# Optimization experiments

Hardware: AMD Instinct MI355X
Metric: run time of the kernel (lower is better)

The kernel has to match this reference:

```python
import jax, jax.numpy as jnp
import numpy as np


def setup_inputs() -> dict:
    key = jax.random.key(0)
    k1, k2 = jax.random.split(key)
    X = jax.random.normal(k1, (8192, 10000), dtype=jnp.float32)
    # logits parameter, xavier_normal init: std = sqrt(2/(fan_in+fan_out))
    std = np.sqrt(2.0 / (256 + 10000)).astype(np.float32)
    logits = jax.random.normal(k2, (256, 10000), dtype=jnp.float32) * std
    return {"X": X, "logits": logits, "temp": 1}


def reference(X, logits, temp):
    # Gumbel-softmax with hard=True (straight-through), matching F.gumbel_softmax.
    gkey = jax.random.key(42)
    g = jax.random.gumbel(gkey, logits.shape, dtype=logits.dtype)
    y_soft = jax.nn.softmax((logits + g) / temp, axis=-1)          # [S, D]
    idx = jnp.argmax(y_soft, axis=-1)                               # [S]
    y_hard = jax.nn.one_hot(idx, logits.shape[-1], dtype=y_soft.dtype)
    # hard forward, soft backward: y_hard - sg(y_soft) + y_soft
    selections = y_hard - jax.lax.stop_gradient(y_soft) + y_soft    # [S, D]
    # Y = X @ selections^T  (one-hot rows -> column gather of X)
    Y = jnp.matmul(X, selections.T)                                 # [B, S]
    return Y
```

## Files before the change

### kernel.cpp

```cpp
#include <hip/hip_runtime.h>
#include <stdint.h>

#define PRNG_VARIANT 1

#define S_ROWS 256
#define D_COLS 10000
#define B_ROWS 8192
#define HALF_N 1280000u

__device__ __forceinline__ void threefry2x32(uint32_t& x0, uint32_t& x1) {
  const uint32_t k0 = 0u;
  const uint32_t k1 = 42u;
  const uint32_t k2 = 0x1BD11BDAu ^ k0 ^ k1;
  x0 += k0; x1 += k1;
#define TFR(r) { x0 += x1; x1 = (x1 << (r)) | (x1 >> (32 - (r))); x1 ^= x0; }
  TFR(13) TFR(15) TFR(26) TFR(6)   x0 += k1; x1 += k2 + 1u;
  TFR(17) TFR(29) TFR(16) TFR(24)  x0 += k2; x1 += k0 + 2u;
  TFR(13) TFR(15) TFR(26) TFR(6)   x0 += k0; x1 += k1 + 3u;
  TFR(17) TFR(29) TFR(16) TFR(24)  x0 += k1; x1 += k2 + 4u;
  TFR(13) TFR(15) TFR(26) TFR(6)   x0 += k2; x1 += k0 + 5u;
#undef TFR
}

__device__ __forceinline__ uint32_t jax_random_bits(uint32_t i) {
#if PRNG_VARIANT == 0
  uint32_t x0, x1;
  if (i < HALF_N) { x0 = i; x1 = i + HALF_N; }
  else            { x0 = i - HALF_N; x1 = i; }
  threefry2x32(x0, x1);
  return (i < HALF_N) ? x0 : x1;
#else
  uint32_t x0 = 0u;
  uint32_t x1 = i;
  threefry2x32(x0, x1);
#if PRNG_VARIANT == 2
  return x0;
#elif PRNG_VARIANT == 3
  return x1;
#else
  return x0 ^ x1;
#endif
#endif
}

__device__ __forceinline__ double gumbel_from_bits(uint32_t bits) {
  uint32_t fb = (bits >> 9) | 0x3f800000u;
  float u = __uint_as_float(fb) - 1.0f;
  if (u <= 0.0f) u = 1.17549435e-38f;
  double lu = log((double)u);
  return -log(-lu);
}

__global__ __launch_bounds__(256)
void argmax_gumbel_kernel(const float* __restrict__ logits, int* __restrict__ idx_out) {
  const int s   = blockIdx.x;
  const int tid = threadIdx.x;

  double best = -1.0e300;
  int    bi   = 0;
  const int base = s * D_COLS;
  for (int d = tid; d < D_COLS; d += 256) {
    uint32_t bits = jax_random_bits((uint32_t)(base + d));
    double z = (double)logits[base + d] + gumbel_from_bits(bits);
    if (z > best) { best = z; bi = d; }
  }

  __shared__ double sv[256];
  __shared__ int    si[256];
  sv[tid] = best; si[tid] = bi;
  __syncthreads();
  for (int off = 128; off > 0; off >>= 1) {
    if (tid < off) {
      double ov = sv[tid + off]; int oi = si[tid + off];
      if (ov > sv[tid] || (ov == sv[tid] && oi < si[tid])) { sv[tid] = ov; si[tid] = oi; }
    }
    __syncthreads();
  }
  if (tid == 0) idx_out[s] = si[0];
}

#define ROWS_PER_BLOCK 16
__global__ __launch_bounds__(256)
void gather_cols_kernel(const float* __restrict__ X,
                        const int* __restrict__ idx,
                        float* __restrict__ Y) {
  const int s   = threadIdx.x;
  const int col = idx[s];
  const long b0 = (long)blockIdx.x * ROWS_PER_BLOCK;
#pragma unroll
  for (int r = 0; r < ROWS_PER_BLOCK; ++r) {
    const long b = b0 + r;
    Y[b * S_ROWS + s] = X[b * D_COLS + col];
  }
}

extern "C" void kernel_launch(void* const* d_in, const int* in_sizes, int n_in,
                              void* d_out, int out_size, void* d_ws, size_t ws_size,
                              hipStream_t stream) {
  const float* X      = (const float*)d_in[0];
  const float* logits = (const float*)d_in[1];
  float*       Y      = (float*)d_out;
  int*         idx    = (int*)d_ws;

  argmax_gumbel_kernel<<<S_ROWS, 256, 0, stream>>>(logits, idx);
  gather_cols_kernel<<<B_ROWS / ROWS_PER_BLOCK, 256, 0, stream>>>(X, idx, Y);
}
```

Measured before the change: 436.9 us.

## Use float Gumbel argmax with double-precision candidate rescoring, wider blocks

The argmax kernel now computes Gumbel noise with float logf instead of double log, buffers z values in shared memory, and rescores in double only the candidates within a small threshold of the float maximum. Blocks grow to 1024 threads. The gather kernel halves rows per block and separates loads from stores to raise memory-level parallelism. Exactness relies on the threshold covering float error, and the serial rescoring is capped at 64 candidates.

```diff
diff --git a/kernel.cpp b/kernel.cpp
--- a/kernel.cpp
+++ b/kernel.cpp
@@ -1,12 +1,10 @@
 #include <hip/hip_runtime.h>
 #include <stdint.h>
 
-#define PRNG_VARIANT 1
 
 #define S_ROWS 256
 #define D_COLS 10000
 #define B_ROWS 8192
-#define HALF_N 1280000u
 
 __device__ __forceinline__ void threefry2x32(uint32_t& x0, uint32_t& x1) {
   const uint32_t k0 = 0u;
@@ -23,63 +21,88 @@
 }
 
 __device__ __forceinline__ uint32_t jax_random_bits(uint32_t i) {
-#if PRNG_VARIANT == 0
-  uint32_t x0, x1;
-  if (i < HALF_N) { x0 = i; x1 = i + HALF_N; }
-  else            { x0 = i - HALF_N; x1 = i; }
+  uint32_t x0 = 0u, x1 = i;
   threefry2x32(x0, x1);
-  return (i < HALF_N) ? x0 : x1;
-#else
-  uint32_t x0 = 0u;
-  uint32_t x1 = i;
-  threefry2x32(x0, x1);
-#if PRNG_VARIANT == 2
-  return x0;
-#elif PRNG_VARIANT == 3
-  return x1;
-#else
   return x0 ^ x1;
-#endif
-#endif
 }
 
-__device__ __forceinline__ double gumbel_from_bits(uint32_t bits) {
+__device__ __forceinline__ float uniform_from_bits(uint32_t bits) {
   uint32_t fb = (bits >> 9) | 0x3f800000u;
   float u = __uint_as_float(fb) - 1.0f;
   if (u <= 0.0f) u = 1.17549435e-38f;
+  return u;
+}
+
+__device__ __forceinline__ float gumbel_f(uint32_t bits) {
+  float u  = uniform_from_bits(bits);
+  float nl = -logf(u);
+  return -logf(nl);
+}
+
+__device__ __forceinline__ double gumbel_d(uint32_t bits) {
+  float u = uniform_from_bits(bits);
   double lu = log((double)u);
   return -log(-lu);
 }
 
-__global__ __launch_bounds__(256)
+#define ARGMAX_THREADS 1024
+#define CAND_MAX 64
+
+__global__ __launch_bounds__(ARGMAX_THREADS)
 void argmax_gumbel_kernel(const float* __restrict__ logits, int* __restrict__ idx_out) {
   const int s   = blockIdx.x;
   const int tid = threadIdx.x;
+  const int base = s * D_COLS;
 
-  double best = -1.0e300;
-  int    bi   = 0;
-  const int base = s * D_COLS;
-  for (int d = tid; d < D_COLS; d += 256) {
+  __shared__ float zbuf[D_COLS];
+  __shared__ float sv[ARGMAX_THREADS];
+  __shared__ int   si[ARGMAX_THREADS];
+  __shared__ int   n_cand;
+  __shared__ int   cand[CAND_MAX];
+
+  if (tid == 0) n_cand = 0;
+
+  float best = -1.0e30f;
+  int   bi   = 0;
+  for (int d = tid; d < D_COLS; d += ARGMAX_THREADS) {
     uint32_t bits = jax_random_bits((uint32_t)(base + d));
-    double z = (double)logits[base + d] + gumbel_from_bits(bits);
+    float z = logits[base + d] + gumbel_f(bits);
+    zbuf[d] = z;
     if (z > best) { best = z; bi = d; }
   }
-
-  __shared__ double sv[256];
-  __shared__ int    si[256];
   sv[tid] = best; si[tid] = bi;
   __syncthreads();
-  for (int off = 128; off > 0; off >>= 1) {
+  for (int off = ARGMAX_THREADS / 2; off > 0; off >>= 1) {
     if (tid < off) {
-      double ov = sv[tid + off]; int oi = si[tid + off];
+      float ov = sv[tid + off]; int oi = si[tid + off];
       if (ov > sv[tid] || (ov == sv[tid] && oi < si[tid])) { sv[tid] = ov; si[tid] = oi; }
     }
     __syncthreads();
   }
-  if (tid == 0) idx_out[s] = si[0];
+
+  const float thresh = sv[0] - 1.0e-3f;
+  for (int d = tid; d < D_COLS; d += ARGMAX_THREADS) {
+    if (zbuf[d] >= thresh) {
+      int pos = atomicAdd(&n_cand, 1);
+      if (pos < CAND_MAX) cand[pos] = d;
+    }
+  }
+  __syncthreads();
+
+  if (tid == 0) {
+    int    nc   = n_cand < CAND_MAX ? n_cand : CAND_MAX;
+    double bz   = -1.0e300;
+    int    bidx = 0x7fffffff;
+    for (int i = 0; i < nc; ++i) {
+      int d = cand[i];
+      double z = (double)logits[base + d] + gumbel_d(jax_random_bits((uint32_t)(base + d)));
+      if (z > bz || (z == bz && d < bidx)) { bz = z; bidx = d; }
+    }
+    idx_out[s] = bidx;
+  }
 }
 
-#define ROWS_PER_BLOCK 16
+#define ROWS_PER_BLOCK 8
 __global__ __launch_bounds__(256)
 void gather_cols_kernel(const float* __restrict__ X,
                         const int* __restrict__ idx,
@@ -87,11 +110,13 @@
   const int s   = threadIdx.x;
   const int col = idx[s];
   const long b0 = (long)blockIdx.x * ROWS_PER_BLOCK;
+  float v[ROWS_PER_BLOCK];
 #pragma unroll
-  for (int r = 0; r < ROWS_PER_BLOCK; ++r) {
-    const long b = b0 + r;
-    Y[b * S_ROWS + s] = X[b * D_COLS + col];
-  }
+  for (int r = 0; r < ROWS_PER_BLOCK; ++r)
+    v[r] = X[(b0 + r) * D_COLS + col];
+#pragma unroll
+  for (int r = 0; r < ROWS_PER_BLOCK; ++r)
+    Y[(b0 + r) * S_ROWS + s] = v[r];
 }
 
 extern "C" void kernel_launch(void* const* d_in, const int* in_sizes, int n_in,
@@ -102,6 +127,6 @@
   float*       Y      = (float*)d_out;
   int*         idx    = (int*)d_ws;
 
-  argmax_gumbel_kernel<<<S_ROWS, 256, 0, stream>>>(logits, idx);
+  argmax_gumbel_kernel<<<S_ROWS, ARGMAX_THREADS, 0, stream>>>(logits, idx);
   gather_cols_kernel<<<B_ROWS / ROWS_PER_BLOCK, 256, 0, stream>>>(X, idx, Y);
 }
```

Measured after the change: 416.5 us. 1.05x faster.
